# Performance work log

Measured on AMD Instinct MI355X. Metric: run time of the kernel, lower is better.

## Reference

```python
import jax, jax.numpy as jnp
import numpy as np

D_MODEL = 768
D_STATE = 64
D_CONV = 4
HEADDIM = 64
D_INNER = 1536
NHEADS = 24
CONV_DIM = D_INNER + 2 * D_STATE          # 1664
D_IN_PROJ = 2 * D_INNER + 2 * D_STATE + NHEADS  # 3224
NLAYERS = 4
NCLASSES = 10
CHUNK = 64


def layernorm(x, w, b, eps=1e-5):
    m = jnp.mean(x, axis=-1, keepdims=True)
    v = jnp.mean((x - m) ** 2, axis=-1, keepdims=True)
    return (x - m) * jax.lax.rsqrt(v + eps) * w + b


def conv1d_same(x, w, b):
    # x: (B, C_in, T), w: (C_out, C_in, K) odd K, torch 'same' padding
    K = w.shape[2]
    out = jax.lax.conv_general_dilated(x, w, (1,), [(K // 2, K // 2)],
                                       dimension_numbers=('NCH', 'OIH', 'NCH'))
    return out + b[None, :, None]


def dw_causal_conv(x, w, b):
    # x: (B, T, C), w: (C, K) depthwise causal conv (mamba conv1d)
    C = x.shape[-1]
    K = w.shape[1]
    xc = x.transpose(0, 2, 1)  # (B, C, T)
    out = jax.lax.conv_general_dilated(xc, w[:, None, :], (1,), [(K - 1, 0)],
                                       dimension_numbers=('NCH', 'OIH', 'NCH'),
                                       feature_group_count=C)
    return out.transpose(0, 2, 1) + b


def ssd(xs, dt, A, Bm, Cm):
    # Chunked SSD (exact Mamba2 recurrence): h_i = exp(dt_i*A) h_{i-1} + dt_i B_i x_i; y_i = C_i h_i
    # xs: (B,T,H,P), dt: (B,T,H), A: (H,), Bm/Cm: (B,T,N)
    Bb, T, H, P = xs.shape
    Nc = T // CHUNK
    la = (dt * A).reshape(Bb, Nc, CHUNK, H)          # per-step log decay (<=0)
    seg = jnp.cumsum(la, axis=2)                      # (b,c,q,h) inclusive cumulative
    Br = Bm.reshape(Bb, Nc, CHUNK, D_STATE)
    Cr = Cm.reshape(Bb, Nc, CHUNK, D_STATE)
    dtx = (dt[..., None] * xs).reshape(Bb, Nc, CHUNK, H, P)
    # intra-chunk: y_i += sum_{j<=i} (C_i.B_j) exp(seg_i - seg_j) dt_j x_j
    scores = jnp.einsum('bcin,bcjn->bcij', Cr, Br)    # (b,c,i,j)
    diff = seg[:, :, :, None, :] - seg[:, :, None, :, :]  # (b,c,i,j,h)
    mask = jnp.tril(jnp.ones((CHUNK, CHUNK), bool))[None, None, :, :, None]
    att = jnp.exp(jnp.where(mask, diff, -jnp.inf)) * scores[..., None]
    y = jnp.einsum('bcijh,bcjhp->bcihp', att, dtx)
    # per-chunk final state contribution
    dec_to_end = jnp.exp(seg[:, :, -1:, :] - seg)     # (b,c,q,h)
    S = jnp.einsum('bcjh,bcjhp,bcjn->bchpn', dec_to_end, dtx, Br)
    chunk_decay = jnp.exp(seg[:, :, -1, :])           # (b,c,h)
    def step(hst, inp):
        S_c, d_c = inp
        out = hst                                     # state at chunk start
        hst = hst * d_c[:, :, None, None] + S_c
        return hst, out
    h0 = jnp.zeros((Bb, H, P, D_STATE), xs.dtype)
    _, Hstarts = jax.lax.scan(step, h0, (S.transpose(1, 0, 2, 3, 4), chunk_decay.transpose(1, 0, 2)))
    Hstarts = Hstarts.transpose(1, 0, 2, 3, 4)        # (b,c,h,p,n)
    y_inter = jnp.einsum('bcin,bchpn->bcihp', Cr, Hstarts) * jnp.exp(seg)[..., None]
    return (y + y_inter).reshape(Bb, T, H, P)


def mamba2(x, Win, cw, cb, dtb, A_log, Dp, nw, Wout):
    Bb, T, _ = x.shape
    zxbcdt = x @ Win.T                                 # (B,T,3224)
    z = zxbcdt[..., :D_INNER]
    xBC = zxbcdt[..., D_INNER:D_INNER + CONV_DIM]
    dt = jax.nn.softplus(zxbcdt[..., -NHEADS:] + dtb)  # (B,T,H)
    xBC = jax.nn.silu(dw_causal_conv(xBC, cw, cb))
    xs = xBC[..., :D_INNER].reshape(Bb, T, NHEADS, HEADDIM)
    Bm = xBC[..., D_INNER:D_INNER + D_STATE]
    Cm = xBC[..., D_INNER + D_STATE:]
    A = -jnp.exp(A_log)                                # (H,)
    y = ssd(xs, dt, A, Bm, Cm) + Dp[None, None, :, None] * xs
    y = y.reshape(Bb, T, D_INNER)
    y = y * jax.nn.silu(z)                             # gated RMSNorm
    y = y * jax.lax.rsqrt(jnp.mean(y * y, axis=-1, keepdims=True) + 1e-5) * nw
    return y @ Wout.T


def setup_inputs() -> dict:
    key = jax.random.key(0)
    ks = iter(jax.random.split(key, 32))
    def rn(shape, s=0.02):
        return jax.random.normal(next(ks), shape, jnp.float32) * s
    L = NLAYERS
    inp = {
        'x': jax.random.normal(next(ks), (8, 2048, 64), jnp.float32),
        'pc_w': rn((128, 64, 1), 0.1), 'pc_b': jnp.zeros((128,)),
        'c1_w': rn((256, 128, 3), 0.05), 'c1_b': jnp.zeros((256,)),
        'c2_w': rn((256, 128, 9), 0.03), 'c2_b': jnp.zeros((256,)),
        'c3_w': rn((256, 128, 27), 0.02), 'c3_b': jnp.zeros((256,)),
        'in_proj': rn((L, D_IN_PROJ, D_MODEL)),
        'conv_w': rn((L, CONV_DIM, D_CONV), 0.2), 'conv_b': jnp.zeros((L, CONV_DIM)),
        'dt_bias': rn((L, NHEADS), 0.5),
        'A_log': jnp.tile(jnp.log(jnp.arange(1, NHEADS + 1, dtype=jnp.float32)), (L, 1)),
        'D': jnp.ones((L, NHEADS)),
        'norm_w': jnp.ones((L, D_INNER)),
        'out_proj': rn((L, D_MODEL, D_INNER)),
        'ln_w': jnp.ones((L, D_MODEL)), 'ln_b': jnp.zeros((L, D_MODEL)),
        'fn_w': jnp.ones((D_MODEL,)), 'fn_b': jnp.zeros((D_MODEL,)),
        'lo_w': rn((NCLASSES, D_MODEL)), 'lo_b': jnp.zeros((NCLASSES,)),
    }
    return inp


def reference(x, pc_w, pc_b, c1_w, c1_b, c2_w, c2_b, c3_w, c3_b,
              in_proj, conv_w, conv_b, dt_bias, A_log, D, norm_w, out_proj,
              ln_w, ln_b, fn_w, fn_b, lo_w, lo_b):
    xt = x.transpose(0, 2, 1)                                  # (B,64,T)
    h = jax.nn.silu(conv1d_same(xt, pc_w, pc_b))               # (B,128,T); dropout = eval identity
    hc = jnp.concatenate([conv1d_same(h, c1_w, c1_b),
                          conv1d_same(h, c2_w, c2_b),
                          conv1d_same(h, c3_w, c3_b)], axis=1)  # (B,768,T)
    h = jax.nn.silu(hc).transpose(0, 2, 1)                      # (B,T,768)
    for l in range(NLAYERS):
        y = mamba2(h, in_proj[l], conv_w[l], conv_b[l], dt_bias[l],
                   A_log[l], D[l], norm_w[l], out_proj[l])
        h = layernorm(y + h, ln_w[l], ln_b[l])
    h = layernorm(h, fn_w, fn_b)
    return h @ lo_w.T + lo_b
```

## Files before the change

### kernel.cpp

```cpp
#include <hip/hip_runtime.h>
#include <hip/hip_bf16.h>
#include <cstdint>
#include <cmath>

#define B_     8
#define T_     2048
#define BT_    16384
#define DM_    768
#define DI_    1536
#define NH_    24
#define CDIM_  1664
#define DPROJ_ 3224
#define ZXB_   3200
#define TPAD_  2080

typedef __hip_bfloat16 bf16;
typedef __attribute__((ext_vector_type(8))) short short8v;
typedef __attribute__((ext_vector_type(4))) short short4v;
typedef __attribute__((ext_vector_type(4))) float float4v;

__device__ __forceinline__ float b2f(bf16 v){ return __bfloat162float(v); }
__device__ __forceinline__ float bu2f(unsigned short u){ return __uint_as_float((unsigned)u << 16); }
__device__ __forceinline__ float siluf(float x){ return x / (1.f + expf(-x)); }
__device__ __forceinline__ unsigned short f2bu(float x){
  unsigned u = __float_as_uint(x);
  u += 0x7FFFu + ((u >> 16) & 1u);
  return (unsigned short)(u >> 16);
}

__global__ void k_detect(const unsigned short* __restrict__ d, int* __restrict__ flag){
  *flag = (d[0] == 0x3F80) ? 1 : 0;
}

struct PrepSeg { const void* src; void* dst; long srcoff; int mode; int p0; int count; };
struct PrepArgs { PrepSeg seg[34]; int cum[35]; };
__global__ __launch_bounds__(256) void k_prep(PrepArgs a, const int* __restrict__ flag, int total){
  int slot = blockIdx.x*256 + threadIdx.x;
  if (slot >= total) return;
  int s = 0;
  while (slot >= a.cum[s+1]) s++;
  PrepSeg g = a.seg[s];
  int off = (slot - a.cum[s]) << 3;
  int rem = g.count - off;
  const int fl = *flag;
  if (g.mode == 0){
    float* d = (float*)g.dst + off;
    if (fl){
      const unsigned short* sp = (const unsigned short*)g.src + g.srcoff + off;
      if (rem >= 8){
        short8v v = *(const short8v*)sp;
        #pragma unroll
        for (int k=0;k<8;k++) d[k] = bu2f((unsigned short)v[k]);
      } else {
        for (int k=0;k<rem;k++) d[k] = bu2f(sp[k]);
      }
    } else {
      const float* sp = (const float*)g.src + g.srcoff + off;
      if (rem >= 8){
        float4 v0 = *(const float4*)sp, v1 = *(const float4*)(sp+4);
        *(float4*)d = v0; *(float4*)(d+4) = v1;
      } else {
        for (int k=0;k<rem;k++) d[k] = sp[k];
      }
    }
  } else if (g.mode == 1){
    unsigned short* d = (unsigned short*)g.dst + off;
    if (fl){
      const unsigned short* sp = (const unsigned short*)g.src + g.srcoff + off;
      if (rem >= 8) *(short8v*)d = *(const short8v*)sp;
      else for (int k=0;k<rem;k++) d[k] = sp[k];
    } else {
      const float* sp = (const float*)g.src + g.srcoff + off;
      if (rem >= 8){
        short8v o;
        #pragma unroll
        for (int k=0;k<8;k++) o[k] = (short)f2bu(sp[k]);
        *(short8v*)d = o;
      } else for (int k=0;k<rem;k++) d[k] = f2bu(sp[k]);
    }
  } else if (g.mode == 3){
    unsigned short* d = (unsigned short*)g.dst + off;
    if (rem >= 8) *(short8v*)d = (short8v)0;
    else for (int k=0;k<rem;k++) d[k] = 0;
  } else {
    int n = rem >= 8 ? 8 : rem;
    for (int k=0;k<n;k++){
      int e = off + k;
      int kk = e % g.p0, rest = e / g.p0;
      float v = fl ? bu2f(((const unsigned short*)g.src)[e]) : ((const float*)g.src)[e];
      ((unsigned short*)g.dst)[(size_t)kk*32768 + rest] = f2bu(v);
    }
  }
}

__global__ __launch_bounds__(256) void k_pcconv(const float* __restrict__ x,
    const float* __restrict__ pw, const float* __restrict__ pb, unsigned short* __restrict__ hpcb,
    int nblk_main){
  if ((int)blockIdx.x >= nblk_main){
    int idx = (blockIdx.x - nblk_main)*256 + threadIdx.x;
    int c = idx & 127;
    int row = (idx >> 7) & 31;
    int b = idx >> 12;
    int tr = (row < 16) ? row : (2064 + row - 16);
    hpcb[((size_t)b*TPAD_ + tr)*128 + c] = 0;
    return;
  }
  int sub = threadIdx.x >> 7;
  int c = threadIdx.x & 127;
  int tok = blockIdx.x*2 + sub;
  __shared__ float xs[2][64];
  if (c < 64) xs[sub][c] = x[(size_t)tok*64 + c];
  __syncthreads();
  float acc = pb[c];
  #pragma unroll 8
  for (int i=0;i<64;i++) acc += xs[sub][i] * pw[c*64 + i];
  int b = tok >> 11, tr = tok & 2047;
  hpcb[((size_t)b*TPAD_ + 16 + tr)*128 + c] = f2bu(siluf(acc));
}

__device__ __forceinline__ void gll16(const void* g, void* l){
  __builtin_amdgcn_global_load_lds((const __attribute__((address_space(1))) void*)g,
                                   (__attribute__((address_space(3))) void*)l, 16, 0, 0);
}

__global__ __launch_bounds__(256) void k_fconv(const unsigned short* __restrict__ hpcb,
    const unsigned short* __restrict__ wfc,
    const float* __restrict__ b1, const float* __restrict__ b2, const float* __restrict__ b3,
    float* __restrict__ h, unsigned short* __restrict__ hb){
  __shared__ unsigned short As[128*32];
  __shared__ unsigned short Bs[128*32];
  const int tok0 = blockIdx.x << 7;
  const int ntile = blockIdx.y;
  const int g = ntile >> 1;
  const int co0 = (ntile & 1) << 7;
  const int Kg = (g==0) ? 3 : (g==1) ? 9 : 27;
  const int tb = (g==0) ? 0 : (g==1) ? 3 : 12;
  const int koff = Kg >> 1;
  const float* bias = (g==0) ? b1 : (g==1) ? b2 : b3;
  const int b = tok0 >> 11, tr0 = tok0 & 2047;
  const size_t browbase = (size_t)b*TPAD_ + 16 + tr0 - koff;

  const int tid = threadIdx.x, wave = tid >> 6, lane = tid & 63;
  const int wm = (wave & 1) << 6, wn = (wave >> 1) << 6;
  const int sr = (wave << 5) + (lane >> 2);
  const int sc = (lane & 3) << 3;
  char* lA0 = (char*)As + (wave << 11);
  char* lA1 = lA0 + 1024;
  char* lB0 = (char*)Bs + (wave << 11);
  char* lB1 = lB0 + 1024;
  float4v acc[4][4];
  #pragma unroll
  for (int i=0;i<4;i++)
    #pragma unroll
    for (int j=0;j<4;j++) acc[i][j] = (float4v)0.f;
  const int ar = wm + (lane & 15);
  const int br = wn + (lane & 15);
  const int kq = (lane >> 4) << 4;

  for (int k = 0; k < Kg; k++){
    const unsigned short* abase = hpcb + (browbase + k)*128;
    const unsigned short* bbase = wfc + (size_t)(tb + k)*32768 + (size_t)co0*128;
    for (int s = 0; s < 4; s++){
      __syncthreads();
      gll16(abase + (size_t)sr*128      + s*32 + sc, lA0);
      gll16(abase + (size_t)(sr+16)*128 + s*32 + sc, lA1);
      gll16(bbase + (size_t)sr*128      + s*32 + sc, lB0);
      gll16(bbase + (size_t)(sr+16)*128 + s*32 + sc, lB1);
      __syncthreads();
      short8v a[4], bb[4];
      #pragma unroll
      for (int f=0; f<4; f++){
        a[f]  = *(const short8v*)((const char*)As + ((ar + (f<<4)) << 6) + kq);
        bb[f] = *(const short8v*)((const char*)Bs + ((br + (f<<4)) << 6) + kq);
      }
      #pragma unroll
      for (int i=0;i<4;i++)
        #pragma unroll
        for (int j=0;j<4;j++)
          acc[i][j] = __builtin_amdgcn_mfma_f32_16x16x32_bf16(a[i], bb[j], acc[i][j], 0, 0, 0);
    }
  }
  #pragma unroll
  for (int i=0;i<4;i++){
    int row = wm + (i<<4) + ((lane>>4)<<2);
    #pragma unroll
    for (int j=0;j<4;j++){
      int col = wn + (j<<4) + (lane & 15);
      int cc = co0 + col;
      float bv = bias[cc];
      int hcol = g*256 + cc;
      #pragma unroll
      for (int r=0;r<4;r++){
        float o = siluf(acc[i][j][r] + bv);
        size_t idx = (size_t)(tok0 + row + r)*DM_ + hcol;
        h[idx] = o;
        hb[idx] = f2bu(o);
      }
    }
  }
}

template<int ACC>
__global__ __launch_bounds__(256) void k_gemm_mfma(const unsigned short* __restrict__ A,
    const unsigned short* __restrict__ W, float* __restrict__ C, int N, int K){
  __shared__ unsigned short As[128*64];
  __shared__ unsigned short Bs[128*64];
  const int bm = blockIdx.x << 7, bn = blockIdx.y << 7;
  const int tid = threadIdx.x, wave = tid >> 6, lane = tid & 63;
  const int wm = (wave & 1) << 6, wn = (wave >> 1) << 6;
  const int srow = lane >> 3;
  const int schk = lane & 7;
  float4v acc[4][4];
  #pragma unroll
  for (int i=0;i<4;i++)
    #pragma unroll
    for (int j=0;j<4;j++) acc[i][j] = (float4v)0.f;
  const int ar = wm + (lane & 15);
  const int br = wn + (lane & 15);
  const int kqc = lane >> 4;

  const int Kh = K / gridDim.z;
  const int k0b = blockIdx.z * Kh;
  for (int k0 = k0b; k0 < k0b + Kh; k0 += 64){
    __syncthreads();
    #pragma unroll
    for (int r = 0; r < 4; r++){
      int row = (r<<5) + (wave<<3) + srow;
      int cg = schk ^ (row & 7);
      gll16(A + (size_t)(bm+row)*K + k0 + (cg<<3), (char*)As + (r<<12) + (wave<<10));
      gll16(W + (size_t)(bn+row)*K + k0 + (cg<<3), (char*)Bs + (r<<12) + (wave<<10));
    }
    __syncthreads();
    #pragma unroll
    for (int ks = 0; ks < 2; ks++){
      short8v a[4], b[4];
      #pragma unroll
      for (int f=0; f<4; f++){
        int rowa = ar + (f<<4);
        int ca = ((ks<<2) + kqc) ^ (rowa & 7);
        a[f] = *(const short8v*)((const char*)As + (rowa<<7) + (ca<<4));
        int rowb = br + (f<<4);
        int cb = ((ks<<2) + kqc) ^ (rowb & 7);
        b[f] = *(const short8v*)((const char*)Bs + (rowb<<7) + (cb<<4));
      }
      #pragma unroll
      for (int i=0;i<4;i++)
        #pragma unroll
        for (int j=0;j<4;j++)
          acc[i][j] = __builtin_amdgcn_mfma_f32_16x16x32_bf16(a[i], b[j], acc[i][j], 0, 0, 0);
    }
  }
  #pragma unroll
  for (int i=0;i<4;i++){
    int row = bm + wm + (i<<4) + ((lane>>4)<<2);
    #pragma unroll
    for (int j=0;j<4;j++){
      int col = bn + wn + (j<<4) + (lane & 15);
      if (col < N){
        #pragma unroll
        for (int r=0;r<4;r++){
          if (ACC) atomicAdd(&C[(size_t)(row+r)*N + col], acc[i][j][r]);
          else     C[(size_t)(row+r)*N + col] = acc[i][j][r];
        }
      }
    }
  }
}

__global__ __launch_bounds__(256) void k_gemm0dt(const unsigned short* __restrict__ A,
    const unsigned short* __restrict__ W, unsigned short* __restrict__ C,
    const float* __restrict__ hs, const float* __restrict__ wdt,
    const float* __restrict__ dtb, const float* __restrict__ Alog,
    float* __restrict__ dtO, float* __restrict__ segO){
  __shared__ __align__(16) char smem[32768];
  if ((int)blockIdx.y < 25){
    unsigned short* As = (unsigned short*)smem;
    unsigned short* Bs = (unsigned short*)(smem + 16384);
    const int bm = blockIdx.x << 7, bn = blockIdx.y << 7;
    const int tid = threadIdx.x, wave = tid >> 6, lane = tid & 63;
    const int wm = (wave & 1) << 6, wn = (wave >> 1) << 6;
    const int srow = lane >> 3;
    const int schk = lane & 7;
    float4v acc[4][4];
    #pragma unroll
    for (int i=0;i<4;i++)
      #pragma unroll
      for (int j=0;j<4;j++) acc[i][j] = (float4v)0.f;
    const int ar = wm + (lane & 15);
    const int br = wn + (lane & 15);
    const int kqc = lane >> 4;
    for (int k0 = 0; k0 < DM_; k0 += 64){
      __syncthreads();
      #pragma unroll
      for (int r = 0; r < 4; r++){
        int row = (r<<5) + (wave<<3) + srow;
        int cg = schk ^ (row & 7);
        gll16(A + (size_t)(bm+row)*DM_ + k0 + (cg<<3), (char*)As + (r<<12) + (wave<<10));
        gll16(W + (size_t)(bn+row)*DM_ + k0 + (cg<<3), (char*)Bs + (r<<12) + (wave<<10));
      }
      __syncthreads();
      #pragma unroll
      for (int ks = 0; ks < 2; ks++){
        short8v a[4], b[4];
        #pragma unroll
        for (int f=0; f<4; f++){
          int rowa = ar + (f<<4);
          int ca = ((ks<<2) + kqc) ^ (rowa & 7);
          a[f] = *(const short8v*)((const char*)As + (rowa<<7) + (ca<<4));
          int rowb = br + (f<<4);
          int cb = ((ks<<2) + kqc) ^ (rowb & 7);
          b[f] = *(const short8v*)((const char*)Bs + (rowb<<7) + (cb<<4));
        }
        #pragma unroll
        for (int i=0;i<4;i++)
          #pragma unroll
          for (int j=0;j<4;j++)
            acc[i][j] = __builtin_amdgcn_mfma_f32_16x16x32_bf16(a[i], b[j], acc[i][j], 0, 0, 0);
      }
    }
    __syncthreads();
    unsigned short* Cs = (unsigned short*)smem;
    #pragma unroll
    for (int i=0;i<4;i++){
      int row0 = wm + (i<<4) + ((lane>>4)<<2);
      #pragma unroll
      for (int j=0;j<4;j++){
        int col = wn + (j<<4) + (lane & 15);
        #pragma unroll
        for (int r=0;r<4;r++){
          int row = row0 + r;
          int byt = (col<<1) ^ ((row&7)<<4);
          Cs[(row<<7) + (byt>>1)] = f2bu(acc[i][j][r]);
        }
      }
    }
    __syncthreads();
    #pragma unroll
    for (int it=0; it<8; it++){
      int row = (it<<4) + (tid>>4);
      int ch = tid & 15;
      int byt = (ch<<4) ^ ((row&7)<<4);
      short8v v = *(const short8v*)((const char*)Cs + (row<<8) + byt);
      *(short8v*)(C + (size_t)(bm+row)*ZXB_ + bn + (ch<<3)) = v;
    }
  } else {
    const int hgrp = blockIdx.y - 25;
    float4* ws = (float4*)smem;
    const float4* wsrc = (const float4*)(wdt + (size_t)hgrp*6*DM_);
    for (int idx = threadIdx.x; idx < 6*192; idx += 256) ws[idx] = wsrc[idx];
    __syncthreads();
    const int w = threadIdx.x >> 6, t = threadIdx.x & 63;
    const int chunk = (blockIdx.x << 1) + (w >> 1);
    const int h0 = hgrp*6 + (w & 1)*3;
    const int tok = chunk*64 + t;
    const float4* a = (const float4*)(hs + (size_t)tok*DM_);
    const float4* w0 = ws + (size_t)(w & 1)*3*192;
    float acc0 = 0.f, acc1 = 0.f, acc2 = 0.f;
    #pragma unroll 4
    for (int kb = 0; kb < 192; kb++){
      float4 av = a[kb];
      float4 v0 = w0[kb];
      float4 v1 = w0[192 + kb];
      float4 v2 = w0[384 + kb];
      acc0 += av.x*v0.x + av.y*v0.y + av.z*v0.z + av.w*v0.w;
      acc1 += av.x*v1.x + av.y*v1.y + av.z*v1.z + av.w*v1.w;
      acc2 += av.x*v2.x + av.y*v2.y + av.z*v2.z + av.w*v2.w;
    }
    float accs[3] = {acc0, acc1, acc2};
    #pragma unroll
    for (int j=0;j<3;j++){
      int h = h0 + j;
      float xv = accs[j] + dtb[h];
      float d = (xv > 15.f) ? xv : log1pf(expf(xv));
      dtO[tok*NH_ + h] = d;
      float la = d * (-expf(Alog[h]));
      #pragma unroll
      for (int off=1; off<64; off<<=1){
        float v = __shfl_up(la, off, 64);
        if (t >= off) la += v;
      }
      segO[tok*NH_ + h] = la;
    }
  }
}

__global__ __launch_bounds__(256) void k_dwconv(const unsigned short* __restrict__ zxb,
    const float* __restrict__ cw, const float* __restrict__ cb, unsigned short* __restrict__ xBC){
  __shared__ float xs[67][128];
  const int i0 = blockIdx.x << 6;
  const int c0 = blockIdx.y << 7;
  const int tid = threadIdx.x;
  const bool haloz = (i0 & (T_-1)) == 0;
  for (int idx = tid; idx < 67*32; idx += 256){
    int r = idx >> 5, c4 = (idx & 31) << 2;
    float4 v = {0.f, 0.f, 0.f, 0.f};
    if (r >= 3 || !haloz){
      short4v b4 = *(const short4v*)(zxb + (size_t)(i0 - 3 + r)*ZXB_ + 1536 + c0 + c4);
      v.x = bu2f((unsigned short)b4[0]); v.y = bu2f((unsigned short)b4[1]);
      v.z = bu2f((unsigned short)b4[2]); v.w = bu2f((unsigned short)b4[3]);
    }
    *(float4*)&xs[r][c4] = v;
  }
  __syncthreads();
  const int cc = tid & 127;
  const int c  = c0 + cc;
  const int tg = (tid >> 7) << 5;
  float wv[4];
  #pragma unroll
  for (int k=0;k<4;k++) wv[k] = cw[c*4+k];
  const float bv = cb[c];
  for (int tt = 0; tt < 32; tt++){
    int tok = tg + tt;
    float acc = bv;
    #pragma unroll
    for (int k=0;k<4;k++) acc += xs[tok+k][cc]*wv[k];
    xBC[(size_t)(i0+tok)*CDIM_ + c] = f2bu(siluf(acc));
  }
}

__global__ __launch_bounds__(256) void k_intra(const unsigned short* __restrict__ xBC,
    const float* __restrict__ dt, const float* __restrict__ seg, const float* __restrict__ Dp,
    unsigned short* __restrict__ y, unsigned short* __restrict__ S){
  const int bc = blockIdx.x, h = blockIdx.y;
  const int tok0 = bc*64;
  __shared__ unsigned short Cb[4096];
  __shared__ unsigned short Bb[4096];
  __shared__ unsigned short XbT[4096];
  __shared__ unsigned short BdT[4096];
  __shared__ float segs[64], dts[64], decs[64];
  const int tid = threadIdx.x;
  if (tid < 64){
    segs[tid] = seg[(tok0+tid)*NH_ + h];
    dts[tid]  = dt [(tok0+tid)*NH_ + h];
  }
  __syncthreads();
  if (tid < 64) decs[tid] = expf(segs[63] - segs[tid]);
  __syncthreads();
  for (int idx = tid; idx < 4096; idx += 256){
    int j = idx >> 6, p = idx & 63;
    const unsigned short* row = xBC + (size_t)(tok0+j)*CDIM_;
    int byt = (p<<1) ^ ((j&7)<<4);
    Cb[(j<<6) + (byt>>1)] = row[1600+p];
    Bb[(j<<6) + (byt>>1)] = row[1536+p];
  }
  for (int idx = tid; idx < 4096; idx += 256){
    int pp = ((idx>>9)<<3) + (idx&7);
    int jj = (((idx>>6)&7)<<3) + ((idx>>3)&7);
    const unsigned short* row2 = xBC + (size_t)(tok0+jj)*CDIM_;
    int byt = (jj<<1) ^ ((pp&7)<<4);
    XbT[(pp<<6) + (byt>>1)] = f2bu(dts[jj] * bu2f(row2[h*64+pp]));
    BdT[(pp<<6) + (byt>>1)] = f2bu(decs[jj] * bu2f(row2[1536+pp]));
  }
  __syncthreads();

  const int wv_ = tid >> 6, lane = tid & 63;
  const int lr = lane & 15;
  const int kq16 = (lane >> 4) << 4;
  const int arow = (wv_ << 4) + lr;
  const int ci = (wv_ << 4) + ((lane >> 4) << 2);

  float4v sc4[4];
  #pragma unroll
  for (int tj=0;tj<4;tj++) sc4[tj] = (float4v)0.f;
  short8v aS[2];
  #pragma unroll
  for (int ks=0; ks<2; ks++)
    aS[ks] = *(const short8v*)((const char*)Cb + (arow<<7) + (((ks<<6) + kq16) ^ ((arow&7)<<4)));
  #pragma unroll 4
  for (int tj=0; tj<=wv_; tj++){
    #pragma unroll
    for (int ks=0; ks<2; ks++){
      int brow = (tj<<4) + lr;
      short8v bf = *(const short8v*)((const char*)Bb + (brow<<7) + (((ks<<6) + kq16) ^ ((brow&7)<<4)));
      sc4[tj] = __builtin_amdgcn_mfma_f32_16x16x32_bf16(aS[ks], bf, sc4[tj], 0, 0, 0);
    }
  }
  #pragma unroll
  for (int tj=0;tj<4;tj++){
    #pragma unroll
    for (int r=0;r<4;r++){
      int i = ci + r;
      int j = (tj<<4) + lr;
      float v = (j <= i) ? expf(segs[i]-segs[j]) * sc4[tj][r] : 0.f;
      int byt = (j<<1) ^ ((i&7)<<4);
      Cb[(i<<6) + (byt>>1)] = f2bu(v);
    }
  }
  __syncthreads();

  float4v yv4[4];
  #pragma unroll
  for (int tp=0;tp<4;tp++) yv4[tp] = (float4v)0.f;
  const int nksP = (wv_ >= 2) ? 2 : 1;
  for (int ks=0; ks<nksP; ks++){
    short8v af = *(const short8v*)((const char*)Cb + (arow<<7) + (((ks<<6) + kq16) ^ ((arow&7)<<4)));
    #pragma unroll
    for (int tp=0;tp<4;tp++){
      int brow = (tp<<4) + lr;
      short8v bf = *(const short8v*)((const char*)XbT + (brow<<7) + (((ks<<6) + kq16) ^ ((brow&7)<<4)));
      yv4[tp] = __builtin_amdgcn_mfma_f32_16x16x32_bf16(af, bf, yv4[tp], 0, 0, 0);
    }
  }
  float4v sv4[4];
  #pragma unroll
  for (int tn=0;tn<4;tn++) sv4[tn] = (float4v)0.f;
  #pragma unroll
  for (int ks=0; ks<2; ks++){
    short8v ax = *(const short8v*)((const char*)XbT + (arow<<7) + (((ks<<6) + kq16) ^ ((arow&7)<<4)));
    #pragma unroll
    for (int tn=0;tn<4;tn++){
      int brow = (tn<<4) + lr;
      short8v bf = *(const short8v*)((const char*)BdT + (brow<<7) + (((ks<<6) + kq16) ^ ((brow&7)<<4)));
      sv4[tn] = __builtin_amdgcn_mfma_f32_16x16x32_bf16(ax, bf, sv4[tn], 0, 0, 0);
    }
  }
  const float Dv = Dp[h];
  #pragma unroll
  for (int tp=0;tp<4;tp++){
    #pragma unroll
    for (int r=0;r<4;r++){
      int i = ci + r;
      int p = (tp<<4) + lr;
      float xo = bu2f(xBC[(size_t)(tok0+i)*CDIM_ + h*64 + p]);
      y[(size_t)(tok0+i)*DI_ + h*64 + p] = f2bu(yv4[tp][r] + Dv*xo);
    }
  }
  unsigned short* sbase = S + ((size_t)bc*NH_ + h)*4096;
  #pragma unroll
  for (int tn=0;tn<4;tn++){
    #pragma unroll
    for (int r=0;r<4;r++){
      int p = ci + r;
      int n = (tn<<4) + lr;
      sbase[(p<<6) + n] = f2bu(sv4[tn][r]);
    }
  }
}

__global__ __launch_bounds__(256) void k_scan(unsigned short* __restrict__ S, const float* __restrict__ seg){
  int b = blockIdx.x, h = blockIdx.y;
  int e = blockIdx.z*256 + threadIdx.x;
  float st = 0.f;
  for (int c=0;c<32;c++){
    float cd = expf(seg[(size_t)((b*32+c)*64+63)*NH_ + h]);
    unsigned short* p = S + ((size_t)(b*32+c)*NH_ + h)*4096 + e;
    float v = bu2f(*p);
    *p = f2bu(st);
    st = st*cd + v;
  }
}

__global__ __launch_bounds__(256) void k_inter(const unsigned short* __restrict__ xBC,
    const float* __restrict__ seg, const unsigned short* __restrict__ S, unsigned short* __restrict__ y){
  const int bc = blockIdx.x, h = blockIdx.y, tok0 = bc*64;
  __shared__ unsigned short Cb[4096];
  __shared__ unsigned short Hb[4096];
  __shared__ float segs[64];
  const int tid = threadIdx.x;
  if (tid < 64) segs[tid] = seg[(tok0+tid)*NH_ + h];
  const unsigned short* sbase = S + ((size_t)bc*NH_ + h)*4096;
  for (int idx = tid; idx < 4096; idx += 256){
    int r = idx >> 6, n = idx & 63;
    int byt = (n<<1) ^ ((r&7)<<4);
    Cb[(r<<6) + (byt>>1)] = xBC[(size_t)(tok0+r)*CDIM_ + 1600 + n];
    Hb[(r<<6) + (byt>>1)] = sbase[idx];
  }
  __syncthreads();
  const int wv_ = tid >> 6, lane = tid & 63;
  const int lr = lane & 15;
  const int kq16 = (lane >> 4) << 4;
  const int arow = (wv_ << 4) + lr;
  const int ci = (wv_ << 4) + ((lane >> 4) << 2);
  float4v acc[4];
  #pragma unroll
  for (int tp=0;tp<4;tp++) acc[tp] = (float4v)0.f;
  short8v aC[2];
  #pragma unroll
  for (int ks=0; ks<2; ks++)
    aC[ks] = *(const short8v*)((const char*)Cb + (arow<<7) + (((ks<<6) + kq16) ^ ((arow&7)<<4)));
  #pragma unroll
  for (int ks=0; ks<2; ks++){
    #pragma unroll
    for (int tp=0;tp<4;tp++){
      int brow = (tp<<4) + lr;
      short8v bf = *(const short8v*)((const char*)Hb + (brow<<7) + (((ks<<6) + kq16) ^ ((brow&7)<<4)));
      acc[tp] = __builtin_amdgcn_mfma_f32_16x16x32_bf16(aC[ks], bf, acc[tp], 0, 0, 0);
    }
  }
  float ei[4];
  #pragma unroll
  for (int r=0;r<4;r++) ei[r] = expf(segs[ci+r]);
  #pragma unroll
  for (int tp=0;tp<4;tp++){
    #pragma unroll
    for (int r=0;r<4;r++){
      int i = ci + r;
      int p = (tp<<4) + lr;
      unsigned short* yr = y + (size_t)(tok0+i)*DI_ + h*64 + p;
      *yr = f2bu(bu2f(*yr) + ei[r]*acc[tp][r]);
    }
  }
}

__global__ __launch_bounds__(256) void k_gate(const unsigned short* __restrict__ y,
    const unsigned short* __restrict__ zxb,
    const float* __restrict__ nw, unsigned short* __restrict__ yb16){
  int tok = blockIdx.x;
  const unsigned short* zr = zxb + (size_t)tok*ZXB_;
  const unsigned short* yr = y + (size_t)tok*DI_;
  unsigned short* ob = yb16 + (size_t)tok*DI_;
  float v[6]; float ss = 0.f;
  #pragma unroll
  for (int e=0;e<6;e++){
    int c = threadIdx.x + e*256;
    float z = bu2f(zr[c]);
    float vv = bu2f(yr[c]) * siluf(z);
    v[e] = vv; ss += vv*vv;
  }
  #pragma unroll
  for (int off=32; off; off>>=1) ss += __shfl_down(ss, off, 64);
  __shared__ float red[4];
  int wid = threadIdx.x >> 6;
  if ((threadIdx.x & 63) == 0) red[wid] = ss;
  __syncthreads();
  float tot = red[0]+red[1]+red[2]+red[3];
  float scale = rsqrtf(tot*(1.f/1536.f) + 1e-5f);
  #pragma unroll
  for (int e=0;e<6;e++){
    int c = threadIdx.x + e*256;
    ob[c] = f2bu(v[e]*scale*nw[c]);
  }
}

__global__ __launch_bounds__(256) void k_resln(float* __restrict__ h,
    const float* __restrict__ lw, const float* __restrict__ lb, unsigned short* __restrict__ hb){
  int tok = blockIdx.x;
  float* hr = h + (size_t)tok*DM_;
  unsigned short* hbr = hb + (size_t)tok*DM_;
  float v[3]; float s = 0.f, s2 = 0.f;
  #pragma unroll
  for (int e=0;e<3;e++){
    int c = threadIdx.x + e*256;
    float xv = hr[c];
    v[e] = xv; s += xv; s2 += xv*xv;
  }
  #pragma unroll
  for (int off=32; off; off>>=1){ s += __shfl_down(s, off, 64); s2 += __shfl_down(s2, off, 64); }
  __shared__ float rs[4], rs2[4];
  int wid = threadIdx.x >> 6;
  if ((threadIdx.x & 63)==0){ rs[wid]=s; rs2[wid]=s2; }
  __syncthreads();
  s  = rs[0]+rs[1]+rs[2]+rs[3];
  s2 = rs2[0]+rs2[1]+rs2[2]+rs2[3];
  float mean = s*(1.f/768.f);
  float var  = s2*(1.f/768.f) - mean*mean;
  float inv  = rsqrtf(var + 1e-5f);
  #pragma unroll
  for (int e=0;e<3;e++){
    int c = threadIdx.x + e*256;
    float o = (v[e]-mean)*inv*lw[c] + lb[c];
    hr[c] = o;
    hbr[c] = f2bu(o);
  }
}

__global__ __launch_bounds__(256) void k_final(const float* __restrict__ h, const float* __restrict__ fw,
    const float* __restrict__ fb, const float* __restrict__ low, const float* __restrict__ lob,
    void* __restrict__ out, const int* __restrict__ flag){
  int tok = blockIdx.x;
  const int isbf = *flag;
  const float* hr = h + (size_t)tok*DM_;
  __shared__ float xn[768];
  __shared__ float rs[4], rs2[4];
  float v[3]; float s=0.f, s2=0.f;
  #pragma unroll
  for (int e=0;e<3;e++){
    int c = threadIdx.x + e*256;
    float xv = hr[c];
    v[e] = xv; s += xv; s2 += xv*xv;
  }
  #pragma unroll
  for (int off=32; off; off>>=1){ s += __shfl_down(s, off, 64); s2 += __shfl_down(s2, off, 64); }
  int wid = threadIdx.x >> 6;
  if ((threadIdx.x & 63)==0){ rs[wid]=s; rs2[wid]=s2; }
  __syncthreads();
  s  = rs[0]+rs[1]+rs[2]+rs[3];
  s2 = rs2[0]+rs2[1]+rs2[2]+rs2[3];
  float mean = s*(1.f/768.f);
  float var  = s2*(1.f/768.f) - mean*mean;
  float inv  = rsqrtf(var + 1e-5f);
  #pragma unroll
  for (int e=0;e<3;e++){
    int c = threadIdx.x + e*256;
    xn[c] = (v[e]-mean)*inv*fw[c] + fb[c];
  }
  __syncthreads();
  if (threadIdx.x < 160){
    int cls = threadIdx.x >> 4, sl = threadIdx.x & 15;
    float acc = 0.f;
    const float* wr = low + cls*768;
    for (int k=sl*48; k<sl*48+48; k++) acc += xn[k]*wr[k];
    #pragma unroll
    for (int off=8; off; off>>=1) acc += __shfl_down(acc, off, 16);
    if (sl==0){
      float r = acc + lob[cls];
      if (isbf) ((bf16*)out)[(size_t)tok*10 + cls] = __float2bfloat16(r);
      else      ((float*)out)[(size_t)tok*10 + cls] = r;
    }
  }
}

extern "C" void kernel_launch(void* const* d_in, const int* in_sizes, int n_in,
                              void* d_out, int out_size, void* d_ws, size_t ws_size,
                              hipStream_t stream) {
  (void)n_in; (void)out_size;
  auto rnd = [](size_t b)->size_t{ return (b + 255) & ~(size_t)255; };

  char* ws = (char*)d_ws;
  int* flag = (int*)ws;
  size_t off = 256;

  const int cvt_idx[18] = {0,1,2,4,6,8,10,11,12,13,14,15,17,18,19,20,21,22};
  float* cf[23] = {nullptr};
  for (int k=0;k<18;k++){
    int i = cvt_idx[k];
    cf[i] = (float*)(ws + off);
    off += rnd((size_t)in_sizes[i]*4);
  }
  float* wdtb = (float*)(ws + off); off += rnd((size_t)4*NH_*DM_*4);
  const int NPAD = 3328;
  unsigned short* inpjb = (unsigned short*)(ws + off); off += rnd((size_t)4*NPAD*DM_*2);
  unsigned short* outpb = (unsigned short*)(ws + off); off += rnd((size_t)4*DM_*DI_*2);
  unsigned short* wfc   = (unsigned short*)(ws + off); off += rnd((size_t)39*256*128*2);

  PrepArgs pa;
  int ns = 0;
  pa.cum[0] = 0;
  auto addseg = [&](const void* src, void* dst, long srcoff, int mode, int p0, int count){
    pa.seg[ns] = {src, dst, srcoff, mode, p0, count};
    pa.cum[ns+1] = pa.cum[ns] + ((count + 7) >> 3);
    ns++;
  };
  addseg(d_in[16], outpb, 0, 1, 0, 4*DM_*DI_);
  for (int l=0;l<4;l++)
    addseg(d_in[9], inpjb + (size_t)l*NPAD*DM_, (long)((size_t)l*DPROJ_)*DM_, 1, 0, DPROJ_*DM_);
  addseg(d_in[0], cf[0], 0, 0, 0, in_sizes[0]);
  addseg(d_in[7], wfc + (size_t)12*32768, 0, 2, 27, 256*128*27);
  addseg(d_in[5], wfc + (size_t)3*32768,  0, 2,  9, 256*128*9);
  addseg(d_in[3], wfc,                    0, 2,  3, 256*128*3);
  for (int l=0;l<4;l++)
    addseg(nullptr, inpjb + (size_t)l*NPAD*DM_ + (size_t)DPROJ_*DM_, 0, 3, 0, (NPAD-DPROJ_)*DM_);
  for (int l=0;l<4;l++)
    addseg(d_in[9], wdtb + (size_t)l*NH_*DM_, (long)((size_t)l*DPROJ_ + 3200)*DM_, 0, 0, NH_*DM_);
  for (int k=1;k<18;k++){
    int i = cvt_idx[k];
    addseg(d_in[i], cf[i], 0, 0, 0, in_sizes[i]);
  }
  int prep_slots = pa.cum[ns];

  const size_t s_h = rnd((size_t)BT_*DM_*4);
  float* h = (float*)(ws + off); off += s_h;
  const size_t s_hb = rnd((size_t)BT_*DM_*2);
  unsigned short* hbf = (unsigned short*)(ws + off); off += s_hb;

  const size_t s_zxb = rnd((size_t)T_*ZXB_*2);
  const size_t s_xbc = rnd((size_t)T_*CDIM_*2);
  const size_t s_dt  = rnd((size_t)T_*NH_*4);
  const size_t s_S   = rnd((size_t)32*NH_*4096*2);
  const size_t s_y   = rnd((size_t)T_*DI_*2);
  const size_t per_batch = s_zxb + s_xbc + 2*s_dt + s_S + s_y;

  size_t remain = (ws_size > off) ? ws_size - off : 0;
  const size_t slack = (size_t)6<<20;
  int nb = 1;
  if (8*per_batch + slack <= remain) nb = 8;
  else if (4*per_batch + slack <= remain) nb = 4;
  else if (2*per_batch + slack <= remain) nb = 2;

  char* arena = ws + off;
  unsigned short* zxb = (unsigned short*)(arena);
  unsigned short* xBC = (unsigned short*)(arena + nb*s_zxb);
  float* dtbuf = (float*)(arena + nb*(s_zxb + s_xbc));
  float* segb  = (float*)(arena + nb*(s_zxb + s_xbc + s_dt));
  unsigned short* Sb = (unsigned short*)(arena + nb*(s_zxb + s_xbc + 2*s_dt));
  unsigned short* yb = (unsigned short*)(arena + nb*(s_zxb + s_xbc + 2*s_dt + s_S));
  unsigned short* ybf = Sb;
  unsigned short* hpcb = (unsigned short*)(arena);

  k_detect<<<1, 1, 0, stream>>>((const unsigned short*)d_in[14], flag);
  k_prep<<<(prep_slots+255)/256, 256, 0, stream>>>(pa, flag, prep_slots);

  k_pcconv<<<BT_/2 + 128, 256, 0, stream>>>(cf[0], cf[1], cf[2], hpcb, BT_/2);
  k_fconv<<<dim3(BT_/128, 6), 256, 0, stream>>>(hpcb, wfc, cf[4], cf[6], cf[8], h, hbf);

  const int nseg = 8 / nb;
  const int ntok = nb * T_;
  const int nch  = nb * 32;

  for (int s = 0; s < nseg; s++){
    float* hs = h + (size_t)s*ntok*DM_;
    unsigned short* hbs = hbf + (size_t)s*ntok*DM_;
    for (int l = 0; l < 4; l++){
      k_gemm0dt<<<dim3(ntok/128, 29), 256, 0, stream>>>(hbs, inpjb + (size_t)l*NPAD*DM_, zxb,
          hs, wdtb + (size_t)l*NH_*DM_, cf[12] + l*NH_, cf[13] + l*NH_, dtbuf, segb);
      k_dwconv<<<dim3(ntok/64, 13), 256, 0, stream>>>(zxb, cf[10] + (size_t)l*CDIM_*4, cf[11] + (size_t)l*CDIM_, xBC);
      k_intra<<<dim3(nch, 24), 256, 0, stream>>>(xBC, dtbuf, segb, cf[14] + l*NH_, yb, Sb);
      k_scan<<<dim3(nb, 24, 16), 256, 0, stream>>>(Sb, segb);
      k_inter<<<dim3(nch, 24), 256, 0, stream>>>(xBC, segb, Sb, yb);
      k_gate<<<ntok, 256, 0, stream>>>(yb, zxb, cf[15] + (size_t)l*DI_, ybf);
      k_gemm_mfma<1><<<dim3(ntok/128, 6, 2), 256, 0, stream>>>(ybf, outpb + (size_t)l*DM_*DI_, hs, DM_, DI_);
      k_resln<<<ntok, 256, 0, stream>>>(hs, cf[17] + l*DM_, cf[18] + l*DM_, hbs);
    }
  }
  k_final<<<BT_, 256, 0, stream>>>(h, cf[19], cf[20], cf[21], cf[22], d_out, flag);
}
```

Before: 2.408 ms.

## Double-buffer LDS tiles in MFMA GEMM kernels to overlap loads with compute

Both bf16 MFMA GEMM kernels (the generic one and the fused in_proj/dt one) now keep two LDS tile buffers. The next K-tile is prefetched with global-to-LDS loads while MFMAs run on the current tile, so each iteration needs one barrier instead of two. The aim is to hide global memory latency behind compute. The cost is double the LDS per block (64 KB), which lowers occupancy. The compiler may also insert wait counts that serialize the async loads anyway.

Measured after the change: 2.341 ms (median of 2 runs). -2.8%, faster.

```diff
diff --git a/kernel.cpp b/kernel.cpp
--- a/kernel.cpp
+++ b/kernel.cpp
@@ -203,8 +203,8 @@
 template<int ACC>
 __global__ __launch_bounds__(256) void k_gemm_mfma(const unsigned short* __restrict__ A,
     const unsigned short* __restrict__ W, float* __restrict__ C, int N, int K){
-  __shared__ unsigned short As[128*64];
-  __shared__ unsigned short Bs[128*64];
+  __shared__ unsigned short As[2][128*64];
+  __shared__ unsigned short Bs[2][128*64];
   const int bm = blockIdx.x << 7, bn = blockIdx.y << 7;
   const int tid = threadIdx.x, wave = tid >> 6, lane = tid & 63;
   const int wm = (wave & 1) << 6, wn = (wave >> 1) << 6;
@@ -221,16 +221,23 @@
 
   const int Kh = K / gridDim.z;
   const int k0b = blockIdx.z * Kh;
-  for (int k0 = k0b; k0 < k0b + Kh; k0 += 64){
-    __syncthreads();
+  const int nt = Kh >> 6;
+
+  auto STAGE = [&](int buf, int k0){
     #pragma unroll
     for (int r = 0; r < 4; r++){
       int row = (r<<5) + (wave<<3) + srow;
       int cg = schk ^ (row & 7);
-      gll16(A + (size_t)(bm+row)*K + k0 + (cg<<3), (char*)As + (r<<12) + (wave<<10));
-      gll16(W + (size_t)(bn+row)*K + k0 + (cg<<3), (char*)Bs + (r<<12) + (wave<<10));
-    }
+      gll16(A + (size_t)(bm+row)*K + k0 + (cg<<3), (char*)As[buf] + (r<<12) + (wave<<10));
+      gll16(W + (size_t)(bn+row)*K + k0 + (cg<<3), (char*)Bs[buf] + (r<<12) + (wave<<10));
+    }
+  };
+
+  STAGE(0, k0b);
+  int cur = 0;
+  for (int t = 0; t < nt; t++){
     __syncthreads();
+    if (t + 1 < nt) STAGE(cur^1, k0b + ((t+1)<<6));
     #pragma unroll
     for (int ks = 0; ks < 2; ks++){
       short8v a[4], b[4];
@@ -238,10 +245,10 @@
       for (int f=0; f<4; f++){
         int rowa = ar + (f<<4);
         int ca = ((ks<<2) + kqc) ^ (rowa & 7);
-        a[f] = *(const short8v*)((const char*)As + (rowa<<7) + (ca<<4));
+        a[f] = *(const short8v*)((const char*)As[cur] + (rowa<<7) + (ca<<4));
         int rowb = br + (f<<4);
         int cb = ((ks<<2) + kqc) ^ (rowb & 7);
-        b[f] = *(const short8v*)((const char*)Bs + (rowb<<7) + (cb<<4));
+        b[f] = *(const short8v*)((const char*)Bs[cur] + (rowb<<7) + (cb<<4));
       }
       #pragma unroll
       for (int i=0;i<4;i++)
@@ -249,6 +256,7 @@
         for (int j=0;j<4;j++)
           acc[i][j] = __builtin_amdgcn_mfma_f32_16x16x32_bf16(a[i], b[j], acc[i][j], 0, 0, 0);
     }
+    cur ^= 1;
   }
   #pragma unroll
   for (int i=0;i<4;i++){
@@ -272,10 +280,8 @@
     const float* __restrict__ hs, const float* __restrict__ wdt,
     const float* __restrict__ dtb, const float* __restrict__ Alog,
     float* __restrict__ dtO, float* __restrict__ segO){
-  __shared__ __align__(16) char smem[32768];
+  __shared__ __align__(16) char smem[65536];
   if ((int)blockIdx.y < 25){
-    unsigned short* As = (unsigned short*)smem;
-    unsigned short* Bs = (unsigned short*)(smem + 16384);
     const int bm = blockIdx.x << 7, bn = blockIdx.y << 7;
     const int tid = threadIdx.x, wave = tid >> 6, lane = tid & 63;
     const int wm = (wave & 1) << 6, wn = (wave >> 1) << 6;
@@ -289,16 +295,23 @@
     const int ar = wm + (lane & 15);
     const int br = wn + (lane & 15);
     const int kqc = lane >> 4;
-    for (int k0 = 0; k0 < DM_; k0 += 64){
-      __syncthreads();
+
+    auto STAGE = [&](int buf, int k0){
       #pragma unroll
       for (int r = 0; r < 4; r++){
         int row = (r<<5) + (wave<<3) + srow;
         int cg = schk ^ (row & 7);
-        gll16(A + (size_t)(bm+row)*DM_ + k0 + (cg<<3), (char*)As + (r<<12) + (wave<<10));
-        gll16(W + (size_t)(bn+row)*DM_ + k0 + (cg<<3), (char*)Bs + (r<<12) + (wave<<10));
-      }
+        gll16(A + (size_t)(bm+row)*DM_ + k0 + (cg<<3), smem + (buf<<14) + (r<<12) + (wave<<10));
+        gll16(W + (size_t)(bn+row)*DM_ + k0 + (cg<<3), smem + 32768 + (buf<<14) + (r<<12) + (wave<<10));
+      }
+    };
+
+    STAGE(0, 0);
+    int cur = 0;
+    const int nt = DM_ >> 6;
+    for (int t = 0; t < nt; t++){
       __syncthreads();
+      if (t + 1 < nt) STAGE(cur^1, (t+1)<<6);
       #pragma unroll
       for (int ks = 0; ks < 2; ks++){
         short8v a[4], b[4];
@@ -306,10 +319,10 @@
         for (int f=0; f<4; f++){
           int rowa = ar + (f<<4);
           int ca = ((ks<<2) + kqc) ^ (rowa & 7);
-          a[f] = *(const short8v*)((const char*)As + (rowa<<7) + (ca<<4));
+          a[f] = *(const short8v*)(smem + (cur<<14) + (rowa<<7) + (ca<<4));
           int rowb = br + (f<<4);
           int cb = ((ks<<2) + kqc) ^ (rowb & 7);
-          b[f] = *(const short8v*)((const char*)Bs + (rowb<<7) + (cb<<4));
+          b[f] = *(const short8v*)(smem + 32768 + (cur<<14) + (rowb<<7) + (cb<<4));
         }
         #pragma unroll
         for (int i=0;i<4;i++)
@@ -317,6 +330,7 @@
           for (int j=0;j<4;j++)
             acc[i][j] = __builtin_amdgcn_mfma_f32_16x16x32_bf16(a[i], b[j], acc[i][j], 0, 0, 0);
       }
+      cur ^= 1;
     }
     __syncthreads();
     unsigned short* Cs = (unsigned short*)smem;
```

## Enlarge MFMA GEMM block tile to 256x128 and widen dt projection per block

Applied to the files above, without the earlier changes.

Both the in-projection GEMM and the out-projection GEMM now use a 256-row by 128-column block tile. Each wave owns 64 rows across the full 128 columns (4x8 MFMA accumulators), which improves reuse of the shared B tile and halves the grid in M. The in-projection epilogue writes the bf16 output through shared memory in two halves. The dt/segment side path now has each wave compute all six heads for its own chunk, doubling the chunks covered per block to match the halved grid. The larger tile uses twice the accumulator registers and more LDS, which can lower occupancy, and the smaller grid may underfill the CUs.

Result: slower. 2.731 ms (+13.4%).

```diff
diff --git a/kernel.cpp b/kernel.cpp
--- a/kernel.cpp
+++ b/kernel.cpp
@@ -203,59 +203,64 @@
 template<int ACC>
 __global__ __launch_bounds__(256) void k_gemm_mfma(const unsigned short* __restrict__ A,
     const unsigned short* __restrict__ W, float* __restrict__ C, int N, int K){
-  __shared__ unsigned short As[128*64];
+  __shared__ unsigned short As[256*64];
   __shared__ unsigned short Bs[128*64];
-  const int bm = blockIdx.x << 7, bn = blockIdx.y << 7;
+  const int bm = blockIdx.x << 8, bn = blockIdx.y << 7;
   const int tid = threadIdx.x, wave = tid >> 6, lane = tid & 63;
-  const int wm = (wave & 1) << 6, wn = (wave >> 1) << 6;
-  const int srow = lane >> 3;
-  const int schk = lane & 7;
-  float4v acc[4][4];
+  const int srow = lane >> 3, schk = lane & 7;
+  const int lr = lane & 15;
+  const int kqc = lane >> 4;
+  float4v acc[4][8];
   #pragma unroll
   for (int i=0;i<4;i++)
     #pragma unroll
-    for (int j=0;j<4;j++) acc[i][j] = (float4v)0.f;
-  const int ar = wm + (lane & 15);
-  const int br = wn + (lane & 15);
-  const int kqc = lane >> 4;
+    for (int j=0;j<8;j++) acc[i][j] = (float4v)0.f;
 
   const int Kh = K / gridDim.z;
   const int k0b = blockIdx.z * Kh;
   for (int k0 = k0b; k0 < k0b + Kh; k0 += 64){
     __syncthreads();
     #pragma unroll
+    for (int r = 0; r < 8; r++){
+      int row = (wave<<6) + (r<<3) + srow;
+      int cg = schk ^ (row & 7);
+      gll16(A + (size_t)(bm+row)*K + k0 + (cg<<3), (char*)As + (wave<<13) + (r<<10));
+    }
+    #pragma unroll
     for (int r = 0; r < 4; r++){
       int row = (r<<5) + (wave<<3) + srow;
       int cg = schk ^ (row & 7);
-      gll16(A + (size_t)(bm+row)*K + k0 + (cg<<3), (char*)As + (r<<12) + (wave<<10));
       gll16(W + (size_t)(bn+row)*K + k0 + (cg<<3), (char*)Bs + (r<<12) + (wave<<10));
     }
     __syncthreads();
     #pragma unroll
     for (int ks = 0; ks < 2; ks++){
-      short8v a[4], b[4];
+      short8v a[4], b[8];
       #pragma unroll
       for (int f=0; f<4; f++){
-        int rowa = ar + (f<<4);
+        int rowa = (wave<<6) + (f<<4) + lr;
         int ca = ((ks<<2) + kqc) ^ (rowa & 7);
         a[f] = *(const short8v*)((const char*)As + (rowa<<7) + (ca<<4));
-        int rowb = br + (f<<4);
+      }
+      #pragma unroll
+      for (int f=0; f<8; f++){
+        int rowb = (f<<4) + lr;
         int cb = ((ks<<2) + kqc) ^ (rowb & 7);
         b[f] = *(const short8v*)((const char*)Bs + (rowb<<7) + (cb<<4));
       }
       #pragma unroll
       for (int i=0;i<4;i++)
         #pragma unroll
-        for (int j=0;j<4;j++)
+        for (int j=0;j<8;j++)
           acc[i][j] = __builtin_amdgcn_mfma_f32_16x16x32_bf16(a[i], b[j], acc[i][j], 0, 0, 0);
     }
   }
   #pragma unroll
   for (int i=0;i<4;i++){
-    int row = bm + wm + (i<<4) + ((lane>>4)<<2);
-    #pragma unroll
-    for (int j=0;j<4;j++){
-      int col = bn + wn + (j<<4) + (lane & 15);
+    int row = bm + (wave<<6) + (i<<4) + ((lane>>4)<<2);
+    #pragma unroll
+    for (int j=0;j<8;j++){
+      int col = bn + (j<<4) + lr;
       if (col < N){
         #pragma unroll
         for (int r=0;r<4;r++){
@@ -272,76 +277,88 @@
     const float* __restrict__ hs, const float* __restrict__ wdt,
     const float* __restrict__ dtb, const float* __restrict__ Alog,
     float* __restrict__ dtO, float* __restrict__ segO){
-  __shared__ __align__(16) char smem[32768];
+  __shared__ __align__(16) char smem[49152];
   if ((int)blockIdx.y < 25){
     unsigned short* As = (unsigned short*)smem;
-    unsigned short* Bs = (unsigned short*)(smem + 16384);
-    const int bm = blockIdx.x << 7, bn = blockIdx.y << 7;
+    unsigned short* Bs = (unsigned short*)(smem + 32768);
+    const int bm = blockIdx.x << 8, bn = blockIdx.y << 7;
     const int tid = threadIdx.x, wave = tid >> 6, lane = tid & 63;
-    const int wm = (wave & 1) << 6, wn = (wave >> 1) << 6;
-    const int srow = lane >> 3;
-    const int schk = lane & 7;
-    float4v acc[4][4];
+    const int srow = lane >> 3, schk = lane & 7;
+    const int lr = lane & 15;
+    const int kqc = lane >> 4;
+    float4v acc[4][8];
     #pragma unroll
     for (int i=0;i<4;i++)
       #pragma unroll
-      for (int j=0;j<4;j++) acc[i][j] = (float4v)0.f;
-    const int ar = wm + (lane & 15);
-    const int br = wn + (lane & 15);
-    const int kqc = lane >> 4;
+      for (int j=0;j<8;j++) acc[i][j] = (float4v)0.f;
+
     for (int k0 = 0; k0 < DM_; k0 += 64){
       __syncthreads();
+      #pragma unroll
+      for (int r = 0; r < 8; r++){
+        int row = (wave<<6) + (r<<3) + srow;
+        int cg = schk ^ (row & 7);
+        gll16(A + (size_t)(bm+row)*DM_ + k0 + (cg<<3), (char*)As + (wave<<13) + (r<<10));
+      }
       #pragma unroll
       for (int r = 0; r < 4; r++){
         int row = (r<<5) + (wave<<3) + srow;
         int cg = schk ^ (row & 7);
-        gll16(A + (size_t)(bm+row)*DM_ + k0 + (cg<<3), (char*)As + (r<<12) + (wave<<10));
         gll16(W + (size_t)(bn+row)*DM_ + k0 + (cg<<3), (char*)Bs + (r<<12) + (wave<<10));
       }
       __syncthreads();
       #pragma unroll
       for (int ks = 0; ks < 2; ks++){
-        short8v a[4], b[4];
+        short8v a[4], b[8];
         #pragma unroll
         for (int f=0; f<4; f++){
-          int rowa = ar + (f<<4);
+          int rowa = (wave<<6) + (f<<4) + lr;
           int ca = ((ks<<2) + kqc) ^ (rowa & 7);
           a[f] = *(const short8v*)((const char*)As + (rowa<<7) + (ca<<4));
-          int rowb = br + (f<<4);
+        }
+        #pragma unroll
+        for (int f=0; f<8; f++){
+          int rowb = (f<<4) + lr;
           int cb = ((ks<<2) + kqc) ^ (rowb & 7);
           b[f] = *(const short8v*)((const char*)Bs + (rowb<<7) + (cb<<4));
         }
         #pragma unroll
         for (int i=0;i<4;i++)
           #pragma unroll
-          for (int j=0;j<4;j++)
+          for (int j=0;j<8;j++)
             acc[i][j] = __builtin_amdgcn_mfma_f32_16x16x32_bf16(a[i], b[j], acc[i][j], 0, 0, 0);
       }
     }
     __syncthreads();
     unsigned short* Cs = (unsigned short*)smem;
     #pragma unroll
-    for (int i=0;i<4;i++){
-      int row0 = wm + (i<<4) + ((lane>>4)<<2);
-      #pragma unroll
-      for (int j=0;j<4;j++){
-        int col = wn + (j<<4) + (lane & 15);
+    for (int half=0; half<2; half++){
+      if ((wave >> 1) == half){
         #pragma unroll
-        for (int r=0;r<4;r++){
-          int row = row0 + r;
-          int byt = (col<<1) ^ ((row&7)<<4);
-          Cs[(row<<7) + (byt>>1)] = f2bu(acc[i][j][r]);
+        for (int i=0;i<4;i++){
+          int lrow0 = ((wave&1)<<6) + (i<<4) + ((lane>>4)<<2);
+          #pragma unroll
+          for (int j=0;j<8;j++){
+            int col = (j<<4) + lr;
+            #pragma unroll
+            for (int r=0;r<4;r++){
+              int lrow = lrow0 + r;
+              int byt = (col<<1) ^ ((lrow&7)<<4);
+              Cs[(lrow<<7) + (byt>>1)] = f2bu(acc[i][j][r]);
+            }
+          }
         }
       }
-    }
-    __syncthreads();
-    #pragma unroll
-    for (int it=0; it<8; it++){
-      int row = (it<<4) + (tid>>4);
-      int ch = tid & 15;
-      int byt = (ch<<4) ^ ((row&7)<<4);
-      short8v v = *(const short8v*)((const char*)Cs + (row<<8) + byt);
-      *(short8v*)(C + (size_t)(bm+row)*ZXB_ + bn + (ch<<3)) = v;
+      __syncthreads();
+      #pragma unroll
+      for (int it=0; it<8; it++){
+        int row = (it<<4) + (tid>>4);
+        int ch = tid & 15;
+        int byt = (ch<<4) ^ ((row&7)<<4);
+        short8v v = *(const short8v*)((const char*)Cs + (row<<8) + byt);
+        *(short8v*)(C + (size_t)(bm+(half<<7)+row)*ZXB_ + bn + (ch<<3)) = v;
+      }
+      __syncthreads();
     }
   } else {
     const int hgrp = blockIdx.y - 25;
@@ -350,26 +367,24 @@
     for (int idx = threadIdx.x; idx < 6*192; idx += 256) ws[idx] = wsrc[idx];
     __syncthreads();
     const int w = threadIdx.x >> 6, t = threadIdx.x & 63;
-    const int chunk = (blockIdx.x << 1) + (w >> 1);
-    const int h0 = hgrp*6 + (w & 1)*3;
+    const int chunk = (blockIdx.x << 2) + w;
     const int tok = chunk*64 + t;
     const float4* a = (const float4*)(hs + (size_t)tok*DM_);
-    const float4* w0 = ws + (size_t)(w & 1)*3*192;
-    float acc0 = 0.f, acc1 = 0.f, acc2 = 0.f;
-    #pragma unroll 4
+    float accs[6];
+    #pragma unroll
+    for (int j=0;j<6;j++) accs[j] = 0.f;
+    #pragma unroll 2
     for (int kb = 0; kb < 192; kb++){
       float4 av = a[kb];
-      float4 v0 = w0[kb];
-      float4 v1 = w0[192 + kb];
-      float4 v2 = w0[384 + kb];
-      acc0 += av.x*v0.x + av.y*v0.y + av.z*v0.z + av.w*v0.w;
-      acc1 += av.x*v1.x + av.y*v1.y + av.z*v1.z + av.w*v1.w;
-      acc2 += av.x*v2.x + av.y*v2.y + av.z*v2.z + av.w*v2.w;
-    }
-    float accs[3] = {acc0, acc1, acc2};
-    #pragma unroll
-    for (int j=0;j<3;j++){
-      int h = h0 + j;
+      #pragma unroll
+      for (int j=0;j<6;j++){
+        float4 v = ws[j*192 + kb];
+        accs[j] += av.x*v.x + av.y*v.y + av.z*v.z + av.w*v.w;
+      }
+    }
+    #pragma unroll
+    for (int j=0;j<6;j++){
+      int h = hgrp*6 + j;
       float xv = accs[j] + dtb[h];
       float d = (xv > 15.f) ? xv : log1pf(expf(xv));
       dtO[tok*NH_ + h] = d;
@@ -801,14 +816,14 @@
     float* hs = h + (size_t)s*ntok*DM_;
     unsigned short* hbs = hbf + (size_t)s*ntok*DM_;
     for (int l = 0; l < 4; l++){
-      k_gemm0dt<<<dim3(ntok/128, 29), 256, 0, stream>>>(hbs, inpjb + (size_t)l*NPAD*DM_, zxb,
+      k_gemm0dt<<<dim3(ntok/256, 29), 256, 0, stream>>>(hbs, inpjb + (size_t)l*NPAD*DM_, zxb,
           hs, wdtb + (size_t)l*NH_*DM_, cf[12] + l*NH_, cf[13] + l*NH_, dtbuf, segb);
       k_dwconv<<<dim3(ntok/64, 13), 256, 0, stream>>>(zxb, cf[10] + (size_t)l*CDIM_*4, cf[11] + (size_t)l*CDIM_, xBC);
       k_intra<<<dim3(nch, 24), 256, 0, stream>>>(xBC, dtbuf, segb, cf[14] + l*NH_, yb, Sb);
       k_scan<<<dim3(nb, 24, 16), 256, 0, stream>>>(Sb, segb);
       k_inter<<<dim3(nch, 24), 256, 0, stream>>>(xBC, segb, Sb, yb);
       k_gate<<<ntok, 256, 0, stream>>>(yb, zxb, cf[15] + (size_t)l*DI_, ybf);
-      k_gemm_mfma<1><<<dim3(ntok/128, 6, 2), 256, 0, stream>>>(ybf, outpb + (size_t)l*DM_*DI_, hs, DM_, DI_);
+      k_gemm_mfma<1><<<dim3(ntok/256, 6, 2), 256, 0, stream>>>(ybf, outpb + (size_t)l*DM_*DI_, hs, DM_, DI_);
       k_resln<<<ntok, 256, 0, stream>>>(hs, cf[17] + l*DM_, cf[18] + l*DM_, hbs);
     }
   }
```
